# Performance work log

Measured on AMD Instinct MI355X. Metric: run time of the kernel, lower is better.

Reference implementation:

```python
import jax, jax.numpy as jnp
import numpy as np

IN_FEATURES = 512
OUT_FEATURES = 512
GRID_SIZE = 5
SPLINE_ORDER = 3
GRID_RANGE = (-3.0, 3.0)


def make_grid():
    h = (GRID_RANGE[1] - GRID_RANGE[0]) / GRID_SIZE
    g = jnp.arange(-SPLINE_ORDER, GRID_SIZE + SPLINE_ORDER + 1, dtype=jnp.float32) * h + GRID_RANGE[0]
    return jnp.broadcast_to(g, (IN_FEATURES, g.shape[0]))  # [in, grid_size+2*order+1]


def b_splines(x, grid):
    # x: [N, in] -> bases: [N, in, grid_size + spline_order]
    x = x[..., None]  # [N, in, 1]
    bases = ((x >= grid[:, :-1]) & (x < grid[:, 1:])).astype(x.dtype)
    for k in range(1, SPLINE_ORDER + 1):
        left = (x - grid[:, :-(k + 1)]) / (grid[:, k:-1] - grid[:, :-(k + 1)])
        right = (grid[:, k + 1:] - x) / (grid[:, k + 1:] - grid[:, 1:-k])
        bases = left * bases[..., :-1] + right * bases[..., 1:]
    return bases


def setup_inputs() -> dict:
    key = jax.random.key(0)
    k1, k2, k3, k4 = jax.random.split(key, 4)
    N = 32768
    bound = 1.0 / np.sqrt(IN_FEATURES)  # kaiming_uniform-ish scale
    x = jax.random.normal(k1, (N, IN_FEATURES), dtype=jnp.float32)
    base_weight = jax.random.uniform(k2, (OUT_FEATURES, IN_FEATURES), minval=-bound, maxval=bound, dtype=jnp.float32)
    spline_weight = jax.random.normal(k3, (OUT_FEATURES, IN_FEATURES, GRID_SIZE + SPLINE_ORDER), dtype=jnp.float32) * 0.1
    spline_scaler = jax.random.uniform(k4, (OUT_FEATURES, IN_FEATURES), minval=-bound, maxval=bound, dtype=jnp.float32)
    grid = make_grid()
    return {"x": x, "base_weight": base_weight, "spline_weight": spline_weight, "spline_scaler": spline_scaler, "grid": grid}


def reference(x, base_weight, spline_weight, spline_scaler, grid):
    # base branch: SiLU(x) @ W_base^T
    base_out = jnp.einsum('ni,oi->no', jax.nn.silu(x), base_weight)
    # spline branch: Cox-de Boor basis then GEMM with scaled spline weights
    b = b_splines(x, grid)  # [N, in, G+K]
    sw = spline_weight * spline_scaler[..., None]  # [out, in, G+K]
    spline_out = jnp.einsum('nik,oik->no', b, sw)
    return base_out + spline_out
```

## Files before the change

kernel.cpp:

```cpp
#include <hip/hip_runtime.h>

#define NSAMP 32768
#define INF 512
#define OUTF 512
#define NB 8
#define KSP 4096
#define KTOT 4608

typedef __attribute__((ext_vector_type(8))) short bf16x8;
typedef __attribute__((ext_vector_type(4))) float f32x4;

typedef __attribute__((address_space(1))) void gas_void;
typedef __attribute__((address_space(3))) void las_void;
#define GLL16(g, l) __builtin_amdgcn_global_load_lds( \
    (const gas_void*)(g), (las_void*)(l), 16, 0, 0)

#define SCHED_PIN() __builtin_amdgcn_sched_barrier(0)

__device__ __forceinline__ unsigned short f2bf(float f) {
  unsigned int u = __float_as_uint(f);
  u += 0x7fffu + ((u >> 16) & 1u);
  return (unsigned short)(u >> 16);
}

__device__ __forceinline__ unsigned pack_rn(float lo, float hi) {
  return __builtin_amdgcn_perm(__float_as_uint(hi) + 0x8000u,
                               __float_as_uint(lo) + 0x8000u, 0x07060302u);
}

__device__ __forceinline__ uint4 kan_basis_vec(float xv) {
  float t = __builtin_fmaf(xv, 1.0f / 1.2f, 5.5f);
  float cf = floorf(t);
  float u = t - cf;
  int j0 = (int)cf - 3;
  float omu = 1.0f - u;
  float u2 = u * u, u3 = u2 * u;
  float omu2 = omu * omu;
  float w0 = omu2 * omu;
  float w1 = __builtin_fmaf(3.f, u3, __builtin_fmaf(-6.f, u2, 4.f));
  float w2 = __builtin_fmaf(-3.f, u3,
              __builtin_fmaf(3.f, u2, __builtin_fmaf(3.f, u, 1.f)));
  float w3 = u3;
  unsigned P0 = pack_rn(w0, w1);
  unsigned P1 = pack_rn(w2, w3);
  int p = j0 & 1;
  unsigned Q0 = p ? (P0 << 16) : P0;
  unsigned Q1 = p ? __builtin_amdgcn_alignbit(P1, P0, 16) : P1;
  unsigned Q2 = p ? (P1 >> 16) : 0u;
  int D = j0 >> 1;
  uint4 r;
  r.x = (D == 0) ? Q0 : (D == -1) ? Q1 : (D == -2) ? Q2 : 0u;
  r.y = (D == 1) ? Q0 : (D ==  0) ? Q1 : (D == -1) ? Q2 : 0u;
  r.z = (D == 2) ? Q0 : (D ==  1) ? Q1 : (D ==  0) ? Q2 : 0u;
  r.w = (D == 3) ? Q0 : (D ==  2) ? Q1 : (D ==  1) ? Q2 : 0u;
  return r;
}

__global__ __launch_bounds__(256) void kan_prep_w(
    const float* __restrict__ bw, const float* __restrict__ sw,
    const float* __restrict__ sc, unsigned short* __restrict__ W) {
  int idx = blockIdx.x * 256 + threadIdx.x;
  float scv = sc[idx] * (1.0f / 6.0f);
  float4 s0 = ((const float4*)sw)[idx * 2 + 0];
  float4 s1 = ((const float4*)sw)[idx * 2 + 1];
  unsigned short v[8];
  v[0] = f2bf(s0.x * scv); v[1] = f2bf(s0.y * scv);
  v[2] = f2bf(s0.z * scv); v[3] = f2bf(s0.w * scv);
  v[4] = f2bf(s1.x * scv); v[5] = f2bf(s1.y * scv);
  v[6] = f2bf(s1.z * scv); v[7] = f2bf(s1.w * scv);
  int o = idx >> 9, i = idx & 511;
  *(bf16x8*)(W + (size_t)o * KTOT + i * NB) = *(bf16x8*)v;
  W[(size_t)o * KTOT + KSP + i] = f2bf(bw[idx]);
}

__device__ __forceinline__ void mfma_chunk(
    const unsigned short* As, const unsigned short* Bs,
    f32x4 acc[4][8], int wm, int wn, int frow, int quad) {
  const int fr7 = frow & 7;
  #pragma unroll
  for (int ks = 0; ks < 2; ++ks) {
    bf16x8 av[4], bv[8];
    const int sa = ((ks * 4 + quad) ^ fr7) * 8;
    #pragma unroll
    for (int f = 0; f < 4; ++f)
      av[f] = *(const bf16x8*)&As[(wm + f * 16 + frow) * 64 + sa];
    #pragma unroll
    for (int g = 0; g < 8; ++g)
      bv[g] = *(const bf16x8*)&Bs[(wn + g * 16 + frow) * 64 + sa];
    #pragma unroll
    for (int mf = 0; mf < 4; ++mf)
      #pragma unroll
      for (int nf = 0; nf < 8; ++nf)
        acc[mf][nf] = __builtin_amdgcn_mfma_f32_16x16x32_bf16(
            av[mf], bv[nf], acc[mf][nf], 0, 0, 0);
  }
}

__global__ __launch_bounds__(256, 2) void kan_fused(
    const float* __restrict__ x, const unsigned short* __restrict__ W,
    float* __restrict__ out) {
  __shared__ __align__(16) unsigned short As[128 * 64];
  __shared__ __align__(16) unsigned short Bs[2][256 * 64];
  const int tid = threadIdx.x;
  const int wave = tid >> 6;
  const int lane = tid & 63;
  const int frow = lane & 15;
  const int quad = lane >> 4;
  const int lr = lane >> 3;
  const int lc = lane & 7;
  const int mtile = blockIdx.x & 255;
  const int ntile = blockIdx.x >> 8;
  const int wm = (wave & 1) << 6;
  const int wn = (wave >> 1) << 7;

  f32x4 acc[4][8];
  #pragma unroll
  for (int i = 0; i < 4; ++i)
    #pragma unroll
    for (int j = 0; j < 8; ++j)
      acc[i][j] = (f32x4){0.f, 0.f, 0.f, 0.f};

  const unsigned short* bg = W +
      (size_t)(ntile * 256 + wave * 64 + lr) * KTOT + ((lc ^ lr) * 8);
  const float* xb = x + (size_t)mtile * 128 * INF;
  const float* xq = xb + (size_t)(wave * 32 + lr) * INF + lc;

  uint4 bb[4];
  #pragma unroll
  for (int is = 0; is < 8; ++is)
    GLL16(bg + is * 36864, &Bs[0][(wave * 64 + is * 8) * 64]);
  bg += 64;
  #pragma unroll
  for (int is = 0; is < 4; ++is)
    bb[is] = kan_basis_vec(xq[is * 4096]);

  for (int kc = 0; kc < 72; ++kc) {
    #pragma unroll
    for (int is = 0; is < 4; ++is)
      *(uint4*)&As[(wave * 32 + is * 8 + lr) * 64 + ((lc ^ lr) * 8)] = bb[is];
    float xn[4];
    if (kc < 63) {
      #pragma unroll
      for (int is = 0; is < 4; ++is) xn[is] = xq[is * 4096 + (kc + 1) * 8];
    }
    if (kc < 71) {
      #pragma unroll
      for (int is = 0; is < 8; ++is)
        GLL16(bg + is * 36864, &Bs[(kc + 1) & 1][(wave * 64 + is * 8) * 64]);
      bg += 64;
    }
    SCHED_PIN();
    if (kc < 63)      asm volatile("s_waitcnt vmcnt(12) lgkmcnt(0)");
    else if (kc < 71) asm volatile("s_waitcnt vmcnt(8) lgkmcnt(0)");
    else              asm volatile("s_waitcnt vmcnt(0) lgkmcnt(0)");
    __builtin_amdgcn_s_barrier();
    SCHED_PIN();

    __builtin_amdgcn_s_setprio(1);
    mfma_chunk(As, Bs[kc & 1], acc, wm, wn, frow, quad);
    __builtin_amdgcn_s_setprio(0);
    if (kc < 63) {
      #pragma unroll
      for (int is = 0; is < 4; ++is) bb[is] = kan_basis_vec(xn[is]);
    } else if (kc < 71) {
      const int sc = kc + 1 - 64;
      #pragma unroll
      for (int is = 0; is < 4; ++is) {
        const float* xr =
            xb + (size_t)(wave * 32 + is * 8 + lr) * INF + sc * 64 + lc * 8;
        float4 a0 = *(const float4*)xr;
        float4 a1 = *(const float4*)(xr + 4);
        float vv[8] = {a0.x, a0.y, a0.z, a0.w, a1.x, a1.y, a1.z, a1.w};
        float s[8];
        #pragma unroll
        for (int e = 0; e < 8; ++e)
          s[e] = vv[e] * __builtin_amdgcn_rcpf(1.0f + __expf(-vv[e]));
        uint4 pk;
        pk.x = pack_rn(s[0], s[1]);
        pk.y = pack_rn(s[2], s[3]);
        pk.z = pack_rn(s[4], s[5]);
        pk.w = pack_rn(s[6], s[7]);
        bb[is] = pk;
      }
    }
    SCHED_PIN();
    asm volatile("s_waitcnt lgkmcnt(0)");
    __builtin_amdgcn_s_barrier();
    SCHED_PIN();
  }

  const size_t m0 = (size_t)mtile * 128;
  const int n0 = ntile * 256;
  #pragma unroll
  for (int mf = 0; mf < 4; ++mf)
    #pragma unroll
    for (int nf = 0; nf < 8; ++nf)
      #pragma unroll
      for (int r = 0; r < 4; ++r)
        out[(m0 + wm + mf * 16 + quad * 4 + r) * OUTF + (n0 + wn + nf * 16 + frow)] =
            acc[mf][nf][r];
}

__global__ __launch_bounds__(256) void kan_naive(
    const float* __restrict__ x, const float* __restrict__ bw,
    const float* __restrict__ sw, const float* __restrict__ sc,
    float* __restrict__ out) {
  int idx = blockIdx.x * 256 + threadIdx.x;
  int n = idx >> 9, o = idx & 511;
  const float* xr = x + (size_t)n * INF;
  float acc = 0.f;
  for (int i = 0; i < INF; ++i) {
    float xv = xr[i];
    float sil = xv / (1.0f + __expf(-xv));
    float t = (xv + 6.6f) * (1.0f / 1.2f);
    float cf = floorf(t);
    float u = t - cf;
    int j0 = (int)cf - 3;
    float omu = 1.0f - u;
    float u2 = u * u, u3 = u2 * u;
    float w[4];
    w[0] = (1.0f / 6.0f) * omu * omu * omu;
    w[1] = (1.0f / 6.0f) * (3.0f * u3 - 6.0f * u2 + 4.0f);
    w[2] = (1.0f / 6.0f) * (-3.0f * u3 + 3.0f * u2 + 3.0f * u + 1.0f);
    w[3] = (1.0f / 6.0f) * u3;
    int wi = o * INF + i;
    acc += sil * bw[wi];
    float sp = 0.f;
    #pragma unroll
    for (int m = 0; m < 4; ++m) {
      int j = j0 + m;
      if ((unsigned)j < 8u) sp += w[m] * sw[wi * NB + j];
    }
    acc += sp * sc[wi];
  }
  out[idx] = acc;
}

extern "C" void kernel_launch(void* const* d_in, const int* in_sizes, int n_in,
                              void* d_out, int out_size, void* d_ws, size_t ws_size,
                              hipStream_t stream) {
  const float* x  = (const float*)d_in[0];
  const float* bw = (const float*)d_in[1];
  const float* sw = (const float*)d_in[2];
  const float* sc = (const float*)d_in[3];
  float* out = (float*)d_out;

  const size_t wbytes = (size_t)OUTF * KTOT * 2;
  if (ws_size >= wbytes) {
    unsigned short* W = (unsigned short*)d_ws;
    kan_prep_w<<<(OUTF * INF) / 256, 256, 0, stream>>>(bw, sw, sc, W);
    kan_fused<<<(NSAMP / 128) * (OUTF / 256), 256, 0, stream>>>(x, W, out);
  } else {
    kan_naive<<<(NSAMP * OUTF) / 256, 256, 0, stream>>>(x, bw, sw, sc, out);
  }
}
```

Baseline: 261.6 us.

## Split K-chunk into four ping-pong MFMA phases interleaved with LDS reads and basis writes

Restructures the main loop so each 64-wide K chunk runs as four 16-MFMA phases separated by barriers, with LDS fragment loads for the next phase issued before each barrier. The basis and SiLU computation for the next A tile is moved to the last phase and written straight into LDS, removing the register-held bb staging and the separate store at loop top. A prologue fills the first A and B tiles before the loop. This aims at a wave-specialised ping-pong schedule where two co-resident blocks alternate MFMA and memory work. In exchange it adds many more barriers per iteration and a full vmcnt(0) wait on each iteration.

```diff
diff --git a/kernel.cpp b/kernel.cpp
--- a/kernel.cpp
+++ b/kernel.cpp
@@ -14,8 +14,6 @@
 typedef __attribute__((address_space(3))) void las_void;
 #define GLL16(g, l) __builtin_amdgcn_global_load_lds( \
     (const gas_void*)(g), (las_void*)(l), 16, 0, 0)
-
-#define SCHED_PIN() __builtin_amdgcn_sched_barrier(0)
 
 __device__ __forceinline__ unsigned short f2bf(float f) {
   unsigned int u = __float_as_uint(f);
@@ -73,27 +71,14 @@
   W[(size_t)o * KTOT + KSP + i] = f2bf(bw[idx]);
 }
 
-__device__ __forceinline__ void mfma_chunk(
-    const unsigned short* As, const unsigned short* Bs,
-    f32x4 acc[4][8], int wm, int wn, int frow, int quad) {
-  const int fr7 = frow & 7;
+__device__ __forceinline__ void mfma16(
+    f32x4 acc[4][8], const bf16x8 av[4], const bf16x8 bv[4], int nh) {
   #pragma unroll
-  for (int ks = 0; ks < 2; ++ks) {
-    bf16x8 av[4], bv[8];
-    const int sa = ((ks * 4 + quad) ^ fr7) * 8;
-    #pragma unroll
-    for (int f = 0; f < 4; ++f)
-      av[f] = *(const bf16x8*)&As[(wm + f * 16 + frow) * 64 + sa];
-    #pragma unroll
-    for (int g = 0; g < 8; ++g)
-      bv[g] = *(const bf16x8*)&Bs[(wn + g * 16 + frow) * 64 + sa];
-    #pragma unroll
-    for (int mf = 0; mf < 4; ++mf)
-      #pragma unroll
-      for (int nf = 0; nf < 8; ++nf)
-        acc[mf][nf] = __builtin_amdgcn_mfma_f32_16x16x32_bf16(
-            av[mf], bv[nf], acc[mf][nf], 0, 0, 0);
-  }
+  for (int mf = 0; mf < 4; ++mf)
+    #pragma unroll
+    for (int g = 0; g < 4; ++g)
+      acc[mf][nh * 4 + g] = __builtin_amdgcn_mfma_f32_16x16x32_bf16(
+          av[mf], bv[g], acc[mf][nh * 4 + g], 0, 0, 0);
 }
 
 __global__ __launch_bounds__(256, 2) void kan_fused(
@@ -112,6 +97,9 @@
   const int ntile = blockIdx.x >> 8;
   const int wm = (wave & 1) << 6;
   const int wn = (wave >> 1) << 7;
+  const int fr7 = frow & 7;
+  const int sa0 = (quad ^ fr7) * 8;
+  const int sa1 = ((4 + quad) ^ fr7) * 8;
 
   f32x4 acc[4][8];
   #pragma unroll
@@ -123,54 +111,108 @@
   const unsigned short* bg = W +
       (size_t)(ntile * 256 + wave * 64 + lr) * KTOT + ((lc ^ lr) * 8);
   const float* xb = x + (size_t)mtile * 128 * INF;
-  const float* xq = xb + (size_t)(wave * 32 + lr) * INF + lc;
-
-  uint4 bb[4];
-  #pragma unroll
-  for (int is = 0; is < 8; ++is)
-    GLL16(bg + is * 36864, &Bs[0][(wave * 64 + is * 8) * 64]);
-  bg += 64;
+  const float* xp[4];
   #pragma unroll
   for (int is = 0; is < 4; ++is)
-    bb[is] = kan_basis_vec(xq[is * 4096]);
+    xp[is] = xb + (size_t)(wave * 32 + is * 8 + lr) * INF + lc;
+
+  {
+    float xc[4];
+    #pragma unroll
+    for (int is = 0; is < 4; ++is) xc[is] = xp[is][0];
+    #pragma unroll
+    for (int is = 0; is < 8; ++is)
+      GLL16(bg + is * 36864, &Bs[0][(wave * 64 + is * 8) * 64]);
+    bg += 64;
+    #pragma unroll
+    for (int is = 0; is < 4; ++is) {
+      uint4 bb = kan_basis_vec(xc[is]);
+      *(uint4*)&As[(wave * 32 + is * 8 + lr) * 64 + ((lc ^ lr) * 8)] = bb;
+    }
+    asm volatile("s_waitcnt vmcnt(0)");
+    __syncthreads();
+  }
 
   for (int kc = 0; kc < 72; ++kc) {
-    #pragma unroll
-    for (int is = 0; is < 4; ++is)
-      *(uint4*)&As[(wave * 32 + is * 8 + lr) * 64 + ((lc ^ lr) * 8)] = bb[is];
+    const unsigned short* Bc = Bs[kc & 1];
+    unsigned short* Bn = (unsigned short*)Bs[(kc + 1) & 1];
+    bf16x8 av[4], bv[4];
     float xn[4];
+    float4 v0[4], v1[4];
+
     if (kc < 63) {
       #pragma unroll
-      for (int is = 0; is < 4; ++is) xn[is] = xq[is * 4096 + (kc + 1) * 8];
+      for (int is = 0; is < 4; ++is) xn[is] = xp[is][(kc + 1) * 8];
     }
     if (kc < 71) {
       #pragma unroll
       for (int is = 0; is < 8; ++is)
-        GLL16(bg + is * 36864, &Bs[(kc + 1) & 1][(wave * 64 + is * 8) * 64]);
+        GLL16(bg + is * 36864, &Bn[(wave * 64 + is * 8) * 64]);
       bg += 64;
     }
-    SCHED_PIN();
-    if (kc < 63)      asm volatile("s_waitcnt vmcnt(12) lgkmcnt(0)");
-    else if (kc < 71) asm volatile("s_waitcnt vmcnt(8) lgkmcnt(0)");
-    else              asm volatile("s_waitcnt vmcnt(0) lgkmcnt(0)");
-    __builtin_amdgcn_s_barrier();
-    SCHED_PIN();
-
+    #pragma unroll
+    for (int f = 0; f < 4; ++f)
+      av[f] = *(const bf16x8*)&As[(wm + f * 16 + frow) * 64 + sa0];
+    #pragma unroll
+    for (int g = 0; g < 4; ++g)
+      bv[g] = *(const bf16x8*)&Bc[(wn + g * 16 + frow) * 64 + sa0];
+    __builtin_amdgcn_s_barrier();
+    asm volatile("s_waitcnt lgkmcnt(0)");
+    __builtin_amdgcn_sched_barrier(0);
     __builtin_amdgcn_s_setprio(1);
-    mfma_chunk(As, Bs[kc & 1], acc, wm, wn, frow, quad);
+    mfma16(acc, av, bv, 0);
     __builtin_amdgcn_s_setprio(0);
-    if (kc < 63) {
-      #pragma unroll
-      for (int is = 0; is < 4; ++is) bb[is] = kan_basis_vec(xn[is]);
-    } else if (kc < 71) {
-      const int sc = kc + 1 - 64;
+    __builtin_amdgcn_s_barrier();
+
+    #pragma unroll
+    for (int g = 0; g < 4; ++g)
+      bv[g] = *(const bf16x8*)&Bc[(wn + (g + 4) * 16 + frow) * 64 + sa0];
+    __builtin_amdgcn_s_barrier();
+    asm volatile("s_waitcnt lgkmcnt(0)");
+    __builtin_amdgcn_sched_barrier(0);
+    __builtin_amdgcn_s_setprio(1);
+    mfma16(acc, av, bv, 1);
+    __builtin_amdgcn_s_setprio(0);
+    __builtin_amdgcn_s_barrier();
+
+    if (kc >= 63 && kc < 71) {
+      const int scn = kc - 63;
       #pragma unroll
       for (int is = 0; is < 4; ++is) {
         const float* xr =
-            xb + (size_t)(wave * 32 + is * 8 + lr) * INF + sc * 64 + lc * 8;
-        float4 a0 = *(const float4*)xr;
-        float4 a1 = *(const float4*)(xr + 4);
-        float vv[8] = {a0.x, a0.y, a0.z, a0.w, a1.x, a1.y, a1.z, a1.w};
+            xb + (size_t)(wave * 32 + is * 8 + lr) * INF + scn * 64 + lc * 8;
+        v0[is] = *(const float4*)xr;
+        v1[is] = *(const float4*)(xr + 4);
+      }
+    }
+    #pragma unroll
+    for (int f = 0; f < 4; ++f)
+      av[f] = *(const bf16x8*)&As[(wm + f * 16 + frow) * 64 + sa1];
+    #pragma unroll
+    for (int g = 0; g < 4; ++g)
+      bv[g] = *(const bf16x8*)&Bc[(wn + g * 16 + frow) * 64 + sa1];
+    __builtin_amdgcn_s_barrier();
+    asm volatile("s_waitcnt lgkmcnt(0)");
+    __builtin_amdgcn_sched_barrier(0);
+    __builtin_amdgcn_s_setprio(1);
+    mfma16(acc, av, bv, 0);
+    __builtin_amdgcn_s_setprio(0);
+    __builtin_amdgcn_s_barrier();
+
+    #pragma unroll
+    for (int g = 0; g < 4; ++g)
+      bv[g] = *(const bf16x8*)&Bc[(wn + (g + 4) * 16 + frow) * 64 + sa1];
+    if (kc < 63) {
+      #pragma unroll
+      for (int is = 0; is < 4; ++is) {
+        uint4 bb = kan_basis_vec(xn[is]);
+        *(uint4*)&As[(wave * 32 + is * 8 + lr) * 64 + ((lc ^ lr) * 8)] = bb;
+      }
+    } else if (kc < 71) {
+      #pragma unroll
+      for (int is = 0; is < 4; ++is) {
+        float vv[8] = {v0[is].x, v0[is].y, v0[is].z, v0[is].w,
+                       v1[is].x, v1[is].y, v1[is].z, v1[is].w};
         float s[8];
         #pragma unroll
         for (int e = 0; e < 8; ++e)
@@ -180,13 +222,18 @@
         pk.y = pack_rn(s[2], s[3]);
         pk.z = pack_rn(s[4], s[5]);
         pk.w = pack_rn(s[6], s[7]);
-        bb[is] = pk;
+        *(uint4*)&As[(wave * 32 + is * 8 + lr) * 64 + ((lc ^ lr) * 8)] = pk;
       }
     }
-    SCHED_PIN();
+    if (kc < 71)
+      asm volatile("s_waitcnt vmcnt(0)");
+    __builtin_amdgcn_s_barrier();
     asm volatile("s_waitcnt lgkmcnt(0)");
-    __builtin_amdgcn_s_barrier();
-    SCHED_PIN();
+    __builtin_amdgcn_sched_barrier(0);
+    __builtin_amdgcn_s_setprio(1);
+    mfma16(acc, av, bv, 1);
+    __builtin_amdgcn_s_setprio(0);
+    __builtin_amdgcn_s_barrier();
   }
 
   const size_t m0 = (size_t)mtile * 128;
```

Measured after the change: 268.7 us. 2.7% more time.
